# Kernel tuning notes

Measured on AMD Instinct MI355X. Metric: run time of the kernel, lower is better.

Reference implementation:

```python
import jax, jax.numpy as jnp
import numpy as np

T, B, D, S, H, OUT = 365, 2048, 32, 27, 256, 1

def _glorot(key, shape):
    fan_in, fan_out = shape[1], shape[0]
    std = jnp.sqrt(2.0 / (fan_in + fan_out))
    return std * jax.random.normal(key, shape, dtype=jnp.float32)

def setup_inputs() -> dict:
    key = jax.random.key(0)
    ks = jax.random.split(key, 9)
    x_dd = jax.random.normal(ks[0], (T, B, D), dtype=jnp.float32)
    x_s = jax.random.normal(ks[1], (B, S), dtype=jnp.float32)
    weight_ih = _glorot(ks[2], (3 * H, D))
    weight_hh = _glorot(ks[3], (3 * H, H))
    bias = jnp.zeros((3 * H,), dtype=jnp.float32)
    w_in = _glorot(ks[4], (H, S))
    b_in = jnp.zeros((H,), dtype=jnp.float32)
    w_dense = _glorot(ks[5], (OUT, H))
    b_dense = jnp.zeros((OUT,), dtype=jnp.float32)
    return {"x_dd": x_dd, "x_s": x_s, "weight_ih": weight_ih,
            "weight_hh": weight_hh, "bias": bias, "w_in": w_in,
            "b_in": b_in, "w_dense": w_dense, "b_dense": b_dense}

def reference(x_dd, x_s, weight_ih, weight_hh, bias, w_in, b_in, w_dense, b_dense):
    # static input gate, computed once per sample: (B, H)
    i = jax.nn.sigmoid(x_s @ w_in.T + b_in)
    # precompute input projections for all timesteps: (T, B, 3H)
    x_proj = jnp.einsum('tbd,gd->tbg', x_dd, weight_ih) + bias

    def step(state, xp):
        h, c = state
        gates = xp + h @ weight_hh.T  # (B, 3H)
        f, g, o = jnp.split(gates, 3, axis=-1)
        f = jax.nn.sigmoid(f)
        g = jnp.tanh(g)
        o = jax.nn.sigmoid(o)
        c = f * c + i * g
        h = o * jnp.tanh(c)
        return (h, c), None

    init = (jnp.zeros((B, H), dtype=x_dd.dtype), jnp.zeros((B, H), dtype=x_dd.dtype))
    (h_final, _), _ = jax.lax.scan(step, init, x_proj)
    return h_final @ w_dense.T + b_dense  # (B, OUT)
```

## Files before the change

kernel.cpp:

```cpp
#include <hip/hip_runtime.h>

#define TT   365
#define BTOT 2048
#define DIN  32
#define SIN  27
#define HD   256
#define G3   768
#define BLOCK 512
#define ZBUF 4096
#define WIHL_OFF 8192
#define WHH7_OFF (WIHL_OFF + G3*64)
#define SMEM_SZ  (WHH7_OFF + G3*64)
#define L2E  1.442695040888963f

#define WS_WIH  (G3*HD*2)
#define WS_BIAS (WS_WIH + G3*DIN*2)

typedef float  f32x4  __attribute__((ext_vector_type(4)));
typedef short  bf16x8 __attribute__((ext_vector_type(8)));
typedef unsigned int u32x2 __attribute__((ext_vector_type(2)));
typedef unsigned int u32x4 __attribute__((ext_vector_type(4)));

__device__ __forceinline__ unsigned short f2bf(float f) {
  unsigned u = __builtin_bit_cast(unsigned, f);
  u += 0x7fffu + ((u >> 16) & 1u);
  return (unsigned short)(u >> 16);
}
__device__ __forceinline__ float bf2f(unsigned short u) {
  unsigned v = ((unsigned)u) << 16;
  return __builtin_bit_cast(float, v);
}
__device__ __forceinline__ bf16x8 cvt8(f32x4 a, f32x4 c) {
  unsigned c0, c1, c2, c3;
  asm("v_cvt_pk_bf16_f32 %0, %1, %2" : "=v"(c0) : "v"(a[0]), "v"(a[1]));
  asm("v_cvt_pk_bf16_f32 %0, %1, %2" : "=v"(c1) : "v"(a[2]), "v"(a[3]));
  asm("v_cvt_pk_bf16_f32 %0, %1, %2" : "=v"(c2) : "v"(c[0]), "v"(c[1]));
  asm("v_cvt_pk_bf16_f32 %0, %1, %2" : "=v"(c3) : "v"(c[2]), "v"(c[3]));
  u32x4 u = u32x4{c0, c1, c2, c3};
  return __builtin_bit_cast(bf16x8, u);
}

__global__ void prep_kernel(const float* __restrict__ whh, const float* __restrict__ wih,
                            const float* __restrict__ bias,
                            unsigned short* __restrict__ whh_bf,
                            unsigned short* __restrict__ wih_bf,
                            float* __restrict__ bias_s) {
  int stride = gridDim.x * blockDim.x;
  int i0 = blockIdx.x * blockDim.x + threadIdx.x;
  for (int i = i0; i < G3 * HD; i += stride) {
    int row = i >> 8;
    float s = (row >= HD && row < 2 * HD) ? 2.0f * L2E : L2E;
    whh_bf[i] = f2bf(whh[i] * s);
  }
  for (int i = i0; i < G3 * DIN; i += stride) {
    int row = i >> 5;
    float s = (row >= HD && row < 2 * HD) ? 2.0f * L2E : L2E;
    wih_bf[i] = f2bf(wih[i] * s);
  }
  for (int i = i0; i < G3; i += stride) {
    float s = (i >= HD && i < 2 * HD) ? 2.0f * L2E : L2E;
    bias_s[i] = bias[i] * s;
  }
}

__global__ void __launch_bounds__(BLOCK, 2)
ealstm_kernel(const float* __restrict__ x_dd, const float* __restrict__ x_s,
              const float* __restrict__ w_in, const float* __restrict__ b_in,
              const float* __restrict__ w_dense, const float* __restrict__ b_dense,
              const unsigned short* __restrict__ whh_bf,
              const unsigned short* __restrict__ wih_bf,
              const float* __restrict__ bias_s,
              float* __restrict__ out) {
  __shared__ __attribute__((aligned(16))) char sm[SMEM_SZ];
  char* zb    = sm;
  char* wihl  = sm + WIHL_OFF;
  char* whh7l = sm + WHH7_OFF;

  const int tid  = threadIdx.x;
  const int b0   = blockIdx.x * 8;
  const int w    = tid >> 6;
  const int lane = tid & 63;
  const int m    = lane & 15;
  const int q    = lane >> 4;
  const int b    = m & 7;
  const int half = m >> 3;

  for (int i = tid; i < G3 * 4; i += BLOCK) {
    int row = i >> 2, qq = i & 3;
    int rot = ((qq + ((row >> 1) & 3)) & 3) << 4;
    *(bf16x8*)(wihl + row * 64 + rot)  = *(const bf16x8*)(wih_bf + row * DIN + qq * 8);
    *(bf16x8*)(whh7l + row * 64 + rot) =
        *(const bf16x8*)(whh_bf + (size_t)row * HD + 7 * 32 + qq * 8);
  }
  if (tid < 256) *(f32x4*)(zb + tid * 16) = f32x4{0.f, 0.f, 0.f, 0.f};

  const float* xp = x_dd + ((size_t)(b0 + b)) * DIN + q * 8;
  f32x4 xa = *(const f32x4*)xp;
  f32x4 xc = *(const f32x4*)(xp + 4);
  xp += (size_t)BTOT * DIN;

  const int sb0 = w * 16;
  int sbs[6];
  bf16x8 wr[6][7];
  #pragma unroll
  for (int s = 0; s < 6; ++s) {
    int sbase = sb0 + (s >= 3 ? 128 : 0) + (s % 3) * 256;
    sbs[s] = sbase;
    const unsigned short* wp = whh_bf + (size_t)(sbase + m) * HD + q * 8;
    #pragma unroll
    for (int kk = 0; kk < 7; ++kk) wr[s][kk] = *(const bf16x8*)(wp + kk * 32);
  }
  #pragma unroll
  for (int s = 0; s < 6; ++s)
    #pragma unroll
    for (int kk = 0; kk < 7; ++kk)
      asm volatile("" : "+v"(wr[s][kk]));

  const int j0 = sb0 + half * 128 + q * 4;
  float cst[4], ig[4];
  #pragma unroll
  for (int r = 0; r < 4; ++r) {
    int j = j0 + r;
    float a = b_in[j];
    const float* xr = x_s + (size_t)(b0 + b) * SIN;
    const float* wn = w_in + (size_t)j * SIN;
    #pragma unroll
    for (int ss = 0; ss < SIN; ++ss) a += xr[ss] * wn[ss];
    ig[r] = __builtin_amdgcn_rcpf(1.0f + __builtin_amdgcn_exp2f(-a * L2E));
    cst[r] = 0.0f;
  }

  const int swz = b << 4;
  const int wro = ((q + ((m >> 1) & 3)) & 3) << 4;
  const int hrb = b * 512;
  const int hq  = q * 16;
  const int hw  = b * 512 + ((j0 * 2) ^ swz);
  const float* bfp = bias_s + j0;
  const float* bgp = bias_s + 256 + j0;
  const float* bop = bias_s + 512 + j0;

  const f32x4 z4 = f32x4{0.f, 0.f, 0.f, 0.f};
  __syncthreads();

  for (int t = 0; t < TT; ++t) {
    char* zc = zb + (t & 1) * ZBUF;
    char* zn = zb + ((t + 1) & 1) * ZBUF;
    const bool more = (t + 1 < TT);

    f32x4 bf4 = *(const f32x4*)bfp;
    f32x4 bg4 = *(const f32x4*)bgp;
    f32x4 bo4 = *(const f32x4*)bop;

    bf16x8 xf = cvt8(xa, xc);
    f32x4 acc0, acc1, acc2, acc3, acc4, acc5;
    {
      bf16x8 w0 = *(const bf16x8*)(wihl + (sbs[0] + m) * 64 + wro);
      bf16x8 w1 = *(const bf16x8*)(wihl + (sbs[1] + m) * 64 + wro);
      bf16x8 w2 = *(const bf16x8*)(wihl + (sbs[2] + m) * 64 + wro);
      bf16x8 w3 = *(const bf16x8*)(wihl + (sbs[3] + m) * 64 + wro);
      bf16x8 w4 = *(const bf16x8*)(wihl + (sbs[4] + m) * 64 + wro);
      bf16x8 w5 = *(const bf16x8*)(wihl + (sbs[5] + m) * 64 + wro);
      acc0 = __builtin_amdgcn_mfma_f32_16x16x32_bf16(w0, xf, z4, 0, 0, 0);
      acc1 = __builtin_amdgcn_mfma_f32_16x16x32_bf16(w1, xf, z4, 0, 0, 0);
      acc2 = __builtin_amdgcn_mfma_f32_16x16x32_bf16(w2, xf, z4, 0, 0, 0);
      acc3 = __builtin_amdgcn_mfma_f32_16x16x32_bf16(w3, xf, z4, 0, 0, 0);
      acc4 = __builtin_amdgcn_mfma_f32_16x16x32_bf16(w4, xf, z4, 0, 0, 0);
      acc5 = __builtin_amdgcn_mfma_f32_16x16x32_bf16(w5, xf, z4, 0, 0, 0);
    }

    if (more) {
      xa = *(const f32x4*)xp;
      xc = *(const f32x4*)(xp + 4);
      xp += (size_t)BTOT * DIN;
    }

    #pragma unroll
    for (int kk = 0; kk < 7; ++kk) {
      bf16x8 hf = *(const bf16x8*)(zc + hrb + ((kk * 64 + hq) ^ swz));
      acc0 = __builtin_amdgcn_mfma_f32_16x16x32_bf16(wr[0][kk], hf, acc0, 0, 0, 0);
      acc1 = __builtin_amdgcn_mfma_f32_16x16x32_bf16(wr[1][kk], hf, acc1, 0, 0, 0);
      acc2 = __builtin_amdgcn_mfma_f32_16x16x32_bf16(wr[2][kk], hf, acc2, 0, 0, 0);
      acc3 = __builtin_amdgcn_mfma_f32_16x16x32_bf16(wr[3][kk], hf, acc3, 0, 0, 0);
      acc4 = __builtin_amdgcn_mfma_f32_16x16x32_bf16(wr[4][kk], hf, acc4, 0, 0, 0);
      acc5 = __builtin_amdgcn_mfma_f32_16x16x32_bf16(wr[5][kk], hf, acc5, 0, 0, 0);
    }
    {
      bf16x8 hf = *(const bf16x8*)(zc + hrb + ((7 * 64 + hq) ^ swz));
      bf16x8 u0 = *(const bf16x8*)(whh7l + (sbs[0] + m) * 64 + wro);
      bf16x8 u1 = *(const bf16x8*)(whh7l + (sbs[1] + m) * 64 + wro);
      bf16x8 u2 = *(const bf16x8*)(whh7l + (sbs[2] + m) * 64 + wro);
      bf16x8 u3 = *(const bf16x8*)(whh7l + (sbs[3] + m) * 64 + wro);
      bf16x8 u4 = *(const bf16x8*)(whh7l + (sbs[4] + m) * 64 + wro);
      bf16x8 u5 = *(const bf16x8*)(whh7l + (sbs[5] + m) * 64 + wro);
      acc0 = __builtin_amdgcn_mfma_f32_16x16x32_bf16(u0, hf, acc0, 0, 0, 0);
      acc1 = __builtin_amdgcn_mfma_f32_16x16x32_bf16(u1, hf, acc1, 0, 0, 0);
      acc2 = __builtin_amdgcn_mfma_f32_16x16x32_bf16(u2, hf, acc2, 0, 0, 0);
      acc3 = __builtin_amdgcn_mfma_f32_16x16x32_bf16(u3, hf, acc3, 0, 0, 0);
      acc4 = __builtin_amdgcn_mfma_f32_16x16x32_bf16(u4, hf, acc4, 0, 0, 0);
      acc5 = __builtin_amdgcn_mfma_f32_16x16x32_bf16(u5, hf, acc5, 0, 0, 0);
    }

    float h0, h1, h2, h3;
    #pragma unroll
    for (int r = 0; r < 4; ++r) {
      float pf = (half ? acc3[r] : acc0[r]) + bf4[r];
      float pg = (half ? acc4[r] : acc1[r]) + bg4[r];
      float po = (half ? acc5[r] : acc2[r]) + bo4[r];
      float fg = __builtin_amdgcn_rcpf(1.0f + __builtin_amdgcn_exp2f(-pf));
      float gg = 1.0f - 2.0f * __builtin_amdgcn_rcpf(1.0f + __builtin_amdgcn_exp2f(pg));
      float og = __builtin_amdgcn_rcpf(1.0f + __builtin_amdgcn_exp2f(-po));
      float c  = fg * cst[r] + ig[r] * gg;
      cst[r] = c;
      float th = 1.0f - 2.0f * __builtin_amdgcn_rcpf(1.0f + __builtin_amdgcn_exp2f(c * (2.0f * L2E)));
      float hv = og * th;
      if (r == 0) h0 = hv; else if (r == 1) h1 = hv; else if (r == 2) h2 = hv; else h3 = hv;
    }
    unsigned pk0, pk1;
    asm("v_cvt_pk_bf16_f32 %0, %1, %2" : "=v"(pk0) : "v"(h0), "v"(h1));
    asm("v_cvt_pk_bf16_f32 %0, %1, %2" : "=v"(pk1) : "v"(h2), "v"(h3));
    u32x2 pk = u32x2{pk0, pk1};
    *(u32x2*)(zn + hw) = pk;

    __syncthreads();
  }

  if (tid < 64) {
    const char* hb = zb + (TT & 1) * ZBUF;
    int row = tid >> 3, seg = tid & 7;
    float sum = 0.0f;
    #pragma unroll
    for (int jj = 0; jj < 32; ++jj) {
      int j = seg * 32 + jj;
      unsigned short hu = *(const unsigned short*)(hb + row * 512 + ((j * 2) ^ (row << 4)));
      sum += bf2f(hu) * w_dense[j];
    }
    sum += __shfl_xor(sum, 1, 64);
    sum += __shfl_xor(sum, 2, 64);
    sum += __shfl_xor(sum, 4, 64);
    if (seg == 0) out[b0 + row] = sum + b_dense[0];
  }
}

extern "C" void kernel_launch(void* const* d_in, const int* in_sizes, int n_in,
                              void* d_out, int out_size, void* d_ws, size_t ws_size,
                              hipStream_t stream) {
  (void)in_sizes; (void)n_in; (void)out_size; (void)ws_size;
  const float* x_dd = (const float*)d_in[0];
  const float* x_s  = (const float*)d_in[1];
  const float* wih  = (const float*)d_in[2];
  const float* whh  = (const float*)d_in[3];
  const float* bias = (const float*)d_in[4];
  const float* w_in = (const float*)d_in[5];
  const float* b_in = (const float*)d_in[6];
  const float* w_d  = (const float*)d_in[7];
  const float* b_d  = (const float*)d_in[8];
  float* out = (float*)d_out;
  unsigned char* ws = (unsigned char*)d_ws;

  unsigned short* whh_bf = (unsigned short*)ws;
  unsigned short* wih_bf = (unsigned short*)(ws + WS_WIH);
  float*          bias_s = (float*)(ws + WS_BIAS);

  prep_kernel<<<128, 256, 0, stream>>>(whh, wih, bias, whh_bf, wih_bf, bias_s);
  ealstm_kernel<<<BTOT / 8, BLOCK, 0, stream>>>(
      x_dd, x_s, w_in, b_in, w_d, b_d, whh_bf, wih_bf, bias_s, out);
}
```

Measured before the change: 518.9 us.

## Replace per-step block barrier with split-phase LDS flag sync between wave groups

Splits the eight waves into two groups, each owning one contiguous half of the hidden units. Each group first multiplies against its own half of the previous hidden state, then waits on the other group's flag before doing the remaining half. This replaces the per-timestep __syncthreads with workgroup-scope atomic counters and a staggered start, so one group's matmul can overlap the other's gate math. The cost is spin-wait polling with s_sleep, a bounded-spin break that could silently skip a wait, and more complex ordering of LDS writes and reads.

```diff
diff --git a/kernel.cpp b/kernel.cpp
--- a/kernel.cpp
+++ b/kernel.cpp
@@ -39,6 +39,13 @@
   u32x4 u = u32x4{c0, c1, c2, c3};
   return __builtin_bit_cast(bf16x8, u);
 }
+__device__ __forceinline__ void waitflag(int* f, int v) {
+  int spins = 0;
+  while (__hip_atomic_load(f, __ATOMIC_ACQUIRE, __HIP_MEMORY_SCOPE_WORKGROUP) < v) {
+    __builtin_amdgcn_s_sleep(1);
+    if (++spins > (1 << 22)) break;
+  }
+}
 
 __global__ void prep_kernel(const float* __restrict__ whh, const float* __restrict__ wih,
                             const float* __restrict__ bias,
@@ -72,6 +79,7 @@
               const float* __restrict__ bias_s,
               float* __restrict__ out) {
   __shared__ __attribute__((aligned(16))) char sm[SMEM_SZ];
+  __shared__ int flg[2];
   char* zb    = sm;
   char* wihl  = sm + WIHL_OFF;
   char* whh7l = sm + WHH7_OFF;
@@ -84,6 +92,8 @@
   const int q    = lane >> 4;
   const int b    = m & 7;
   const int half = m >> 3;
+  const int grp  = w >> 2;
+  const int wl   = w & 3;
 
   for (int i = tid; i < G3 * 4; i += BLOCK) {
     int row = i >> 2, qq = i & 3;
@@ -93,18 +103,19 @@
         *(const bf16x8*)(whh_bf + (size_t)row * HD + 7 * 32 + qq * 8);
   }
   if (tid < 256) *(f32x4*)(zb + tid * 16) = f32x4{0.f, 0.f, 0.f, 0.f};
+  if (tid == 0) { flg[0] = 0; flg[1] = 0; }
 
   const float* xp = x_dd + ((size_t)(b0 + b)) * DIN + q * 8;
   f32x4 xa = *(const f32x4*)xp;
   f32x4 xc = *(const f32x4*)(xp + 4);
   xp += (size_t)BTOT * DIN;
 
-  const int sb0 = w * 16;
+  const int sb0 = grp * 128 + wl * 32;
   int sbs[6];
   bf16x8 wr[6][7];
   #pragma unroll
   for (int s = 0; s < 6; ++s) {
-    int sbase = sb0 + (s >= 3 ? 128 : 0) + (s % 3) * 256;
+    int sbase = sb0 + (s >= 3 ? 16 : 0) + (s % 3) * 256;
     sbs[s] = sbase;
     const unsigned short* wp = whh_bf + (size_t)(sbase + m) * HD + q * 8;
     #pragma unroll
@@ -116,7 +127,7 @@
     for (int kk = 0; kk < 7; ++kk)
       asm volatile("" : "+v"(wr[s][kk]));
 
-  const int j0 = sb0 + half * 128 + q * 4;
+  const int j0 = sb0 + half * 16 + q * 4;
   float cst[4], ig[4];
   #pragma unroll
   for (int r = 0; r < 4; ++r) {
@@ -138,9 +149,43 @@
   const float* bfp = bias_s + j0;
   const float* bgp = bias_s + 256 + j0;
   const float* bop = bias_s + 512 + j0;
+  int* flgO = &flg[grp];
+  int* flgP = &flg[grp ^ 1];
 
   const f32x4 z4 = f32x4{0.f, 0.f, 0.f, 0.f};
   __syncthreads();
+
+  if (grp) {
+    __builtin_amdgcn_s_sleep(6);
+    __builtin_amdgcn_s_sleep(6);
+    __builtin_amdgcn_s_sleep(6);
+  }
+
+#define H_OCT_REG(KK) do { \
+    bf16x8 hf = *(const bf16x8*)(zc + hrb + (((KK) * 64 + hq) ^ swz)); \
+    acc0 = __builtin_amdgcn_mfma_f32_16x16x32_bf16(wr[0][KK], hf, acc0, 0, 0, 0); \
+    acc1 = __builtin_amdgcn_mfma_f32_16x16x32_bf16(wr[1][KK], hf, acc1, 0, 0, 0); \
+    acc2 = __builtin_amdgcn_mfma_f32_16x16x32_bf16(wr[2][KK], hf, acc2, 0, 0, 0); \
+    acc3 = __builtin_amdgcn_mfma_f32_16x16x32_bf16(wr[3][KK], hf, acc3, 0, 0, 0); \
+    acc4 = __builtin_amdgcn_mfma_f32_16x16x32_bf16(wr[4][KK], hf, acc4, 0, 0, 0); \
+    acc5 = __builtin_amdgcn_mfma_f32_16x16x32_bf16(wr[5][KK], hf, acc5, 0, 0, 0); \
+  } while (0)
+
+#define H_OCT_LDS() do { \
+    bf16x8 hf = *(const bf16x8*)(zc + hrb + ((7 * 64 + hq) ^ swz)); \
+    bf16x8 u0 = *(const bf16x8*)(whh7l + (sbs[0] + m) * 64 + wro); \
+    bf16x8 u1 = *(const bf16x8*)(whh7l + (sbs[1] + m) * 64 + wro); \
+    bf16x8 u2 = *(const bf16x8*)(whh7l + (sbs[2] + m) * 64 + wro); \
+    bf16x8 u3 = *(const bf16x8*)(whh7l + (sbs[3] + m) * 64 + wro); \
+    bf16x8 u4 = *(const bf16x8*)(whh7l + (sbs[4] + m) * 64 + wro); \
+    bf16x8 u5 = *(const bf16x8*)(whh7l + (sbs[5] + m) * 64 + wro); \
+    acc0 = __builtin_amdgcn_mfma_f32_16x16x32_bf16(u0, hf, acc0, 0, 0, 0); \
+    acc1 = __builtin_amdgcn_mfma_f32_16x16x32_bf16(u1, hf, acc1, 0, 0, 0); \
+    acc2 = __builtin_amdgcn_mfma_f32_16x16x32_bf16(u2, hf, acc2, 0, 0, 0); \
+    acc3 = __builtin_amdgcn_mfma_f32_16x16x32_bf16(u3, hf, acc3, 0, 0, 0); \
+    acc4 = __builtin_amdgcn_mfma_f32_16x16x32_bf16(u4, hf, acc4, 0, 0, 0); \
+    acc5 = __builtin_amdgcn_mfma_f32_16x16x32_bf16(u5, hf, acc5, 0, 0, 0); \
+  } while (0)
 
   for (int t = 0; t < TT; ++t) {
     char* zc = zb + (t & 1) * ZBUF;
@@ -167,38 +212,19 @@
       acc4 = __builtin_amdgcn_mfma_f32_16x16x32_bf16(w4, xf, z4, 0, 0, 0);
       acc5 = __builtin_amdgcn_mfma_f32_16x16x32_bf16(w5, xf, z4, 0, 0, 0);
     }
-
     if (more) {
       xa = *(const f32x4*)xp;
       xc = *(const f32x4*)(xp + 4);
       xp += (size_t)BTOT * DIN;
     }
 
-    #pragma unroll
-    for (int kk = 0; kk < 7; ++kk) {
-      bf16x8 hf = *(const bf16x8*)(zc + hrb + ((kk * 64 + hq) ^ swz));
-      acc0 = __builtin_amdgcn_mfma_f32_16x16x32_bf16(wr[0][kk], hf, acc0, 0, 0, 0);
-      acc1 = __builtin_amdgcn_mfma_f32_16x16x32_bf16(wr[1][kk], hf, acc1, 0, 0, 0);
-      acc2 = __builtin_amdgcn_mfma_f32_16x16x32_bf16(wr[2][kk], hf, acc2, 0, 0, 0);
-      acc3 = __builtin_amdgcn_mfma_f32_16x16x32_bf16(wr[3][kk], hf, acc3, 0, 0, 0);
-      acc4 = __builtin_amdgcn_mfma_f32_16x16x32_bf16(wr[4][kk], hf, acc4, 0, 0, 0);
-      acc5 = __builtin_amdgcn_mfma_f32_16x16x32_bf16(wr[5][kk], hf, acc5, 0, 0, 0);
-    }
-    {
-      bf16x8 hf = *(const bf16x8*)(zc + hrb + ((7 * 64 + hq) ^ swz));
-      bf16x8 u0 = *(const bf16x8*)(whh7l + (sbs[0] + m) * 64 + wro);
-      bf16x8 u1 = *(const bf16x8*)(whh7l + (sbs[1] + m) * 64 + wro);
-      bf16x8 u2 = *(const bf16x8*)(whh7l + (sbs[2] + m) * 64 + wro);
-      bf16x8 u3 = *(const bf16x8*)(whh7l + (sbs[3] + m) * 64 + wro);
-      bf16x8 u4 = *(const bf16x8*)(whh7l + (sbs[4] + m) * 64 + wro);
-      bf16x8 u5 = *(const bf16x8*)(whh7l + (sbs[5] + m) * 64 + wro);
-      acc0 = __builtin_amdgcn_mfma_f32_16x16x32_bf16(u0, hf, acc0, 0, 0, 0);
-      acc1 = __builtin_amdgcn_mfma_f32_16x16x32_bf16(u1, hf, acc1, 0, 0, 0);
-      acc2 = __builtin_amdgcn_mfma_f32_16x16x32_bf16(u2, hf, acc2, 0, 0, 0);
-      acc3 = __builtin_amdgcn_mfma_f32_16x16x32_bf16(u3, hf, acc3, 0, 0, 0);
-      acc4 = __builtin_amdgcn_mfma_f32_16x16x32_bf16(u4, hf, acc4, 0, 0, 0);
-      acc5 = __builtin_amdgcn_mfma_f32_16x16x32_bf16(u5, hf, acc5, 0, 0, 0);
-    }
+    waitflag(flgO, 4 * t);
+    if (grp == 0) { H_OCT_REG(0); H_OCT_REG(1); H_OCT_REG(2); H_OCT_REG(3); }
+    else          { H_OCT_REG(4); H_OCT_REG(5); H_OCT_REG(6); H_OCT_LDS(); }
+
+    waitflag(flgP, 4 * t);
+    if (grp == 0) { H_OCT_REG(4); H_OCT_REG(5); H_OCT_REG(6); H_OCT_LDS(); }
+    else          { H_OCT_REG(0); H_OCT_REG(1); H_OCT_REG(2); H_OCT_REG(3); }
 
     float h0, h1, h2, h3;
     #pragma unroll
@@ -221,8 +247,14 @@
     u32x2 pk = u32x2{pk0, pk1};
     *(u32x2*)(zn + hw) = pk;
 
-    __syncthreads();
-  }
+    asm volatile("s_waitcnt lgkmcnt(0)" ::: "memory");
+    if (lane == 0)
+      __hip_atomic_fetch_add(flgO, 1, __ATOMIC_RELEASE, __HIP_MEMORY_SCOPE_WORKGROUP);
+  }
+#undef H_OCT_REG
+#undef H_OCT_LDS
+
+  __syncthreads();
 
   if (tid < 64) {
     const char* hb = zb + (TT & 1) * ZBUF;
```

New measurement: 799.0 us. 1.54x slower.
